# Optimization experiments

Measured on AMD Instinct MI355X. Metric: run time of the kernel, lower is better.

## Reference

```python
import jax, jax.numpy as jnp
import numpy as np

B, S, H = 2, 2048, 2048
NH, G = 16, 4
HD = H // NH  # 128


def setup_inputs() -> dict:
    key = jax.random.key(0)
    ks = jax.random.split(key, 9)
    sc = 0.02
    x = jax.random.normal(ks[0], (B, S, H), dtype=jnp.float32)
    # causal mask: 1.0 where j > i (masked), added as mask * -1e9 (matches torch code)
    causal_mask = jnp.triu(jnp.ones((S, S), dtype=jnp.float32), k=1)[None, None]
    Wq = jax.random.normal(ks[1], (H, H), dtype=jnp.float32) * sc
    bq = jnp.zeros((H,), dtype=jnp.float32)
    Wk = jax.random.normal(ks[2], (H, G * HD), dtype=jnp.float32) * sc
    bk = jnp.zeros((G * HD,), dtype=jnp.float32)
    Wv = jax.random.normal(ks[3], (H, G * HD), dtype=jnp.float32) * sc
    bv = jnp.zeros((G * HD,), dtype=jnp.float32)
    Wo = jax.random.normal(ks[4], (H, H), dtype=jnp.float32) * sc
    bo = jnp.zeros((H,), dtype=jnp.float32)
    return {"hidden_state": x, "causal_mask": causal_mask,
            "Wq": Wq, "bq": bq, "Wk": Wk, "bk": bk,
            "Wv": Wv, "bv": bv, "Wo": Wo, "bo": bo}


def reference(hidden_state, causal_mask, Wq, bq, Wk, bk, Wv, bv, Wo, bo):
    bsz, seq_len, _ = hidden_state.shape
    npg = NH // G  # query heads per KV group
    q = hidden_state @ Wq + bq                      # [B,S,H]
    k = hidden_state @ Wk + bk                      # [B,S,G*HD]
    v = hidden_state @ Wv + bv                      # [B,S,G*HD]
    # split heads; group query heads by KV group instead of repeating K/V
    q = q.reshape(bsz, seq_len, G, npg, HD).transpose(0, 2, 3, 1, 4)   # [B,G,npg,S,HD]
    k = k.reshape(bsz, seq_len, G, HD).transpose(0, 2, 1, 3)           # [B,G,S,HD]
    v = v.reshape(bsz, seq_len, G, HD).transpose(0, 2, 1, 3)           # [B,G,S,HD]
    scale = 1.0 / jnp.sqrt(jnp.float32(HD))
    scores = jnp.einsum('bgnsd,bgtd->bgnst', q, k) * scale             # [B,G,npg,S,S]
    scores = scores + causal_mask[:, :, None] * (-1e9)
    probs = jax.nn.softmax(scores, axis=-1)
    out = jnp.einsum('bgnst,bgtd->bgnsd', probs, v)                    # [B,G,npg,S,HD]
    out = out.transpose(0, 3, 1, 2, 4).reshape(bsz, seq_len, H)        # [B,S,H]
    return out @ Wo + bo
```

## Files before the change

### kernel.cpp

```cpp
#include <hip/hip_runtime.h>
#include <hip/hip_bf16.h>

#define B_   2
#define S_   2048
#define H_   2048
#define NH_  16
#define G_   4
#define HD_  128
#define NPG_ 4
#define MROWS_ (B_ * S_)
#define KVC_   (G_ * HD_)
#define NT_    (S_ / 64)
#define QSCALE_ 0.08838834764831845f

typedef __attribute__((ext_vector_type(8))) short bf16x8;
typedef __attribute__((ext_vector_type(4))) float f32x4;

__device__ __forceinline__ short f2bf_s(float f) {
    __hip_bfloat16 h = __float2bfloat16(f);
    short s; __builtin_memcpy(&s, &h, 2); return s;
}

__device__ __forceinline__ void gll16(const void* g, void* l) {
    __builtin_amdgcn_global_load_lds(
        (const __attribute__((address_space(1))) unsigned int*)g,
        (__attribute__((address_space(3))) unsigned int*)l, 16, 0, 0);
}

struct alignas(16) bf8pack { short s[8]; };
struct alignas(8)  s4pack  { short s[4]; };

__device__ __forceinline__ bf16x8 ld2x64(const short* p) {
    s4pack lo = *(const s4pack*)p;
    s4pack hi = *(const s4pack*)(p + 4);
    bf16x8 v;
    __builtin_memcpy(&v, &lo, 8);
    __builtin_memcpy((char*)&v + 8, &hi, 8);
    return v;
}

__device__ __forceinline__ void tile_transpose(
    const float* __restrict__ in, __hip_bfloat16* __restrict__ out,
    int R, int C, int bx, int by, int tid) {
    __shared__ short tile[32][33];
    int tx = tid & 31, ty0 = tid >> 5;
    #pragma unroll
    for (int i = 0; i < 32; i += 8)
        tile[ty0 + i][tx] = f2bf_s(in[(size_t)(by * 32 + ty0 + i) * C + bx * 32 + tx]);
    __syncthreads();
    #pragma unroll
    for (int i = 0; i < 32; i += 8) {
        short s = tile[tx][ty0 + i];
        __hip_bfloat16 h; __builtin_memcpy(&h, &s, 2);
        out[(size_t)(bx * 32 + ty0 + i) * R + by * 32 + tx] = h;
    }
}

__global__ __launch_bounds__(256) void prep(
    const float* __restrict__ x,  bf8pack* __restrict__ xb,
    const float* __restrict__ Wq, __hip_bfloat16* __restrict__ WqT,
    const float* __restrict__ Wk, __hip_bfloat16* __restrict__ WkT,
    const float* __restrict__ Wv, __hip_bfloat16* __restrict__ WvT,
    const float* __restrict__ Wo, __hip_bfloat16* __restrict__ WoT,
    const float* __restrict__ bq, const float* __restrict__ bk,
    const float* __restrict__ bv, float* __restrict__ bqkv) {
    const int bid = blockIdx.x, tid = threadIdx.x;
    if (bid < 4096) {
        int i = bid * 256 + tid;
        const float4* p = (const float4*)(x + (size_t)i * 8);
        float4 a = p[0], c = p[1];
        bf8pack o;
        o.s[0] = f2bf_s(a.x); o.s[1] = f2bf_s(a.y);
        o.s[2] = f2bf_s(a.z); o.s[3] = f2bf_s(a.w);
        o.s[4] = f2bf_s(c.x); o.s[5] = f2bf_s(c.y);
        o.s[6] = f2bf_s(c.z); o.s[7] = f2bf_s(c.w);
        xb[i] = o;
    } else if (bid < 8192) {
        int t = bid - 4096;
        tile_transpose(Wq, WqT, H_, H_, t & 63, t >> 6, tid);
    } else if (bid < 9216) {
        int t = bid - 8192;
        tile_transpose(Wk, WkT, H_, KVC_, t & 15, t >> 4, tid);
    } else if (bid < 10240) {
        int t = bid - 9216;
        tile_transpose(Wv, WvT, H_, KVC_, t & 15, t >> 4, tid);
    } else if (bid < 14336) {
        int t = bid - 10240;
        tile_transpose(Wo, WoT, H_, H_, t & 63, t >> 6, tid);
    } else {
        int i = (bid - 14336) * 256 + tid;
        if (i < 3072)
            bqkv[i] = (i < 2048) ? bq[i] : (i < 2560) ? bk[i - 2048] : bv[i - 2560];
    }
}

#define GEMM_STAGE(As_, Bs_, Ap_, Bp_, K_)                                   \
    {                                                                        \
        const int lrow = lane >> 3;                                          \
        const int cg = ((lane ^ lrow) & 7) * 8;                              \
        _Pragma("unroll")                                                    \
        for (int p = 0; p < 4; ++p) {                                        \
            int r0 = wave * 32 + p * 8;                                      \
            gll16(Ap_ + (size_t)(bm + r0 + lrow) * K_ + kt + cg,             \
                  &As_[r0 * 64]);                                            \
            gll16(Bp_ + (size_t)(bn + r0 + lrow) * K_ + kt + cg,             \
                  &Bs_[r0 * 64]);                                            \
        }                                                                    \
    }

#define GEMM_MFMA(As_, Bs_)                                                  \
    _Pragma("unroll")                                                        \
    for (int ks = 0; ks < 2; ++ks) {                                         \
        bf16x8 af[4], bfr[4];                                                \
        _Pragma("unroll")                                                    \
        for (int i = 0; i < 4; ++i) {                                        \
            int ra = wm + i * 16 + l15, rb = wn + i * 16 + l15;              \
            af[i]  = *(const bf16x8*)(&As_[ra * 64 +                         \
                          (((ks * 4 + quad) ^ (ra & 7)) * 8)]);              \
            bfr[i] = *(const bf16x8*)(&Bs_[rb * 64 +                         \
                          (((ks * 4 + quad) ^ (rb & 7)) * 8)]);              \
        }                                                                    \
        _Pragma("unroll")                                                    \
        for (int i = 0; i < 4; ++i)                                          \
            _Pragma("unroll")                                                \
            for (int j = 0; j < 4; ++j)                                      \
                acc[i][j] = __builtin_amdgcn_mfma_f32_16x16x32_bf16(         \
                    af[i], bfr[j], acc[i][j], 0, 0, 0);                      \
    }

__global__ __launch_bounds__(256) void gemm_qkv(
    const __hip_bfloat16* __restrict__ A,
    const __hip_bfloat16* __restrict__ Bt,
    const float* __restrict__ bias,
    __hip_bfloat16* __restrict__ Qo,
    __hip_bfloat16* __restrict__ Ko,
    __hip_bfloat16* __restrict__ VtG) {
    __shared__ short As[128 * 64];
    __shared__ short Bs[128 * 64];
    const int K = H_;
    const int t = threadIdx.x;
    const int lane = t & 63, wave = t >> 6;
    const int l15 = lane & 15, quad = lane >> 4;
    const int bm = blockIdx.x * 128, bn = blockIdx.y * 128;
    const int wm = (wave >> 1) * 64, wn = (wave & 1) * 64;

    f32x4 acc[4][4] = {};
    for (int kt = 0; kt < K; kt += 64) {
        GEMM_STAGE(As, Bs, A, Bt, K)
        __syncthreads();
        GEMM_MFMA(As, Bs)
        __syncthreads();
    }

    if (bn < 2560) {
        __hip_bfloat16* Cp; int stride, cb; float scl;
        if (bn < 2048) { Cp = Qo; stride = H_;   cb = bn;        scl = QSCALE_; }
        else           { Cp = Ko; stride = KVC_; cb = bn - 2048; scl = 1.f; }
        #pragma unroll
        for (int i = 0; i < 4; ++i) {
            int row0 = bm + wm + i * 16 + quad * 4;
            #pragma unroll
            for (int j = 0; j < 4; ++j) {
                int colg = bn + wn + j * 16 + l15;
                int coll = cb + wn + j * 16 + l15;
                float bv = bias[colg];
                #pragma unroll
                for (int r = 0; r < 4; ++r)
                    Cp[(size_t)(row0 + r) * stride + coll] =
                        __float2bfloat16((acc[i][j][r] + bv) * scl);
            }
        }
    } else {
        #pragma unroll
        for (int i = 0; i < 4; ++i) {
            int row0 = bm + wm + i * 16 + quad * 4;
            #pragma unroll
            for (int j = 0; j < 4; ++j) {
                int colg = bn + wn + j * 16 + l15;
                int coll = colg - 2560;
                float bv = bias[colg];
                short s4[4];
                #pragma unroll
                for (int r = 0; r < 4; ++r) s4[r] = f2bf_s(acc[i][j][r] + bv);
                *(uint2*)(&VtG[(size_t)coll * MROWS_ + row0]) = *(uint2*)s4;
            }
        }
    }
}

__global__ __launch_bounds__(256) void gemm_out(
    const __hip_bfloat16* __restrict__ A,
    const __hip_bfloat16* __restrict__ Bt,
    const float* __restrict__ bias,
    float* __restrict__ C) {
    __shared__ short As[128 * 64];
    __shared__ short Bs[128 * 64];
    const int K = H_, N = H_;
    const int t = threadIdx.x;
    const int lane = t & 63, wave = t >> 6;
    const int l15 = lane & 15, quad = lane >> 4;
    const int bm = blockIdx.x * 128, bn = blockIdx.y * 128;
    const int wm = (wave >> 1) * 64, wn = (wave & 1) * 64;

    f32x4 acc[4][4] = {};
    for (int kt = 0; kt < K; kt += 64) {
        GEMM_STAGE(As, Bs, A, Bt, K)
        __syncthreads();
        GEMM_MFMA(As, Bs)
        __syncthreads();
    }

    #pragma unroll
    for (int i = 0; i < 4; ++i) {
        int row0 = bm + wm + i * 16 + quad * 4;
        #pragma unroll
        for (int j = 0; j < 4; ++j) {
            int col = bn + wn + j * 16 + l15;
            float bv = bias[col];
            #pragma unroll
            for (int r = 0; r < 4; ++r)
                C[(size_t)(row0 + r) * N + col] = acc[i][j][r] + bv;
        }
    }
}

__global__ __launch_bounds__(256, 2) void attn_causal_gqa(
    const __hip_bfloat16* __restrict__ Q,
    const __hip_bfloat16* __restrict__ K,
    const __hip_bfloat16* __restrict__ VtG,
    __hip_bfloat16* __restrict__ O) {
    __shared__ short KsL[64 * 128];
    __shared__ short VtL[128 * 64];
    __shared__ short Ps[4][2][16 * 72];

    const int h  = blockIdx.x;
    const int b  = h >> 4;
    const int hh = h & 15;
    const int g  = hh >> 2;
    const int qb1 = blockIdx.y;
    const int qb2 = NT_ - 1 - qb1;

    const int t = threadIdx.x;
    const int lane = t & 63, wave = t >> 6;
    const int l15 = lane & 15, quad = lane >> 4;
    const int swz = l15 & 7;

    const __hip_bfloat16* Qb = Q + (size_t)b * S_ * H_ + hh * HD_;
    const __hip_bfloat16* Kb = K + (size_t)b * S_ * KVC_ + g * HD_;
    const __hip_bfloat16* Vg = VtG + (size_t)g * HD_ * MROWS_ + b * S_;

    bf16x8 aq1[4], aq2[4];
    {
        const int qr1 = qb1 * 64 + wave * 16 + l15;
        const int qr2 = qb2 * 64 + wave * 16 + l15;
        #pragma unroll
        for (int kk = 0; kk < 4; ++kk) {
            aq1[kk] = *(const bf16x8*)(Qb + (size_t)qr1 * H_ + kk * 32 + quad * 8);
            aq2[kk] = *(const bf16x8*)(Qb + (size_t)qr2 * H_ + kk * 32 + quad * 8);
        }
    }

    f32x4 o1[8] = {}, o2[8] = {};
    float lp1 = 0.f, lp2 = 0.f;
    const int qrow_loc = wave * 16 + l15;

    for (int tile = 0; tile <= qb2; ++tile) {
        const int key0 = tile * 64;
        const bool do1 = (tile <= qb1);

        #pragma unroll
        for (int p = 0; p < 4; ++p) {
            int R0 = wave * 16 + p * 4;
            int row = R0 + (lane >> 4);
            int cg = ((lane & 15) ^ (row & 7)) * 8;
            gll16(Kb + (size_t)(key0 + row) * KVC_ + cg, &KsL[R0 * 128]);
        }
        #pragma unroll
        for (int p = 0; p < 4; ++p) {
            int R0 = wave * 32 + p * 8;
            int row = R0 + (lane >> 3);
            int cg = ((lane & 7) ^ (row & 7)) * 8;
            gll16(Vg + (size_t)row * MROWS_ + key0 + cg, &VtL[R0 * 64]);
        }
        __syncthreads();

        f32x4 s2[4] = {}, s1[4] = {};
        #pragma unroll
        for (int kk = 0; kk < 4; ++kk) {
            bf16x8 bk[4];
            #pragma unroll
            for (int nt = 0; nt < 4; ++nt)
                bk[nt] = *(const bf16x8*)(
                    &KsL[(nt * 16 + l15) * 128 + (((kk * 4 + quad) ^ swz) * 8)]);
            #pragma unroll
            for (int nt = 0; nt < 4; ++nt)
                s2[nt] = __builtin_amdgcn_mfma_f32_16x16x32_bf16(
                    bk[nt], aq2[kk], s2[nt], 0, 0, 0);
            if (do1) {
                #pragma unroll
                for (int nt = 0; nt < 4; ++nt)
                    s1[nt] = __builtin_amdgcn_mfma_f32_16x16x32_bf16(
                        bk[nt], aq1[kk], s1[nt], 0, 0, 0);
            }
        }

        __asm__ volatile("" ::: "memory");
        short* P2 = &Ps[wave][1][0];
        {
            const bool m2 = (tile == qb2);
            #pragma unroll
            for (int nt = 0; nt < 4; ++nt) {
                s4pack pk;
                #pragma unroll
                for (int r = 0; r < 4; ++r) {
                    float p = __expf(s2[nt][r]);
                    if (m2 && (nt * 16 + quad * 4 + r > qrow_loc)) p = 0.f;
                    lp2 += p;
                    pk.s[r] = f2bf_s(p);
                }
                *(s4pack*)&P2[l15 * 72 + nt * 16 + quad * 4] = pk;
            }
        }
        short* P1 = &Ps[wave][0][0];
        if (do1) {
            const bool m1 = (tile == qb1);
            #pragma unroll
            for (int nt = 0; nt < 4; ++nt) {
                s4pack pk;
                #pragma unroll
                for (int r = 0; r < 4; ++r) {
                    float p = __expf(s1[nt][r]);
                    if (m1 && (nt * 16 + quad * 4 + r > qrow_loc)) p = 0.f;
                    lp1 += p;
                    pk.s[r] = f2bf_s(p);
                }
                *(s4pack*)&P1[l15 * 72 + nt * 16 + quad * 4] = pk;
            }
        }
        __asm__ volatile("" ::: "memory");

        #pragma unroll
        for (int ks = 0; ks < 2; ++ks) {
            bf16x8 ap2 = ld2x64(&P2[l15 * 72 + ks * 32 + quad * 8]);
            bf16x8 ap1;
            if (do1) ap1 = ld2x64(&P1[l15 * 72 + ks * 32 + quad * 8]);
            #pragma unroll
            for (int n2 = 0; n2 < 8; ++n2) {
                bf16x8 bv = *(const bf16x8*)(
                    &VtL[(n2 * 16 + l15) * 64 + (((ks * 4 + quad) ^ swz) * 8)]);
                o2[n2] = __builtin_amdgcn_mfma_f32_16x16x32_bf16(
                    ap2, bv, o2[n2], 0, 0, 0);
                if (do1)
                    o1[n2] = __builtin_amdgcn_mfma_f32_16x16x32_bf16(
                        ap1, bv, o1[n2], 0, 0, 0);
            }
        }
        __syncthreads();
    }

    float L1 = lp1, L2 = lp2;
    L1 += __shfl_xor(L1, 16); L2 += __shfl_xor(L2, 16);
    L1 += __shfl_xor(L1, 32); L2 += __shfl_xor(L2, 32);
    #pragma unroll
    for (int r = 0; r < 4; ++r) {
        float i1 = 1.f / __shfl(L1, quad * 4 + r);
        float i2 = 1.f / __shfl(L2, quad * 4 + r);
        int s1r = qb1 * 64 + wave * 16 + quad * 4 + r;
        int s2r = qb2 * 64 + wave * 16 + quad * 4 + r;
        #pragma unroll
        for (int n2 = 0; n2 < 8; ++n2) {
            int d = n2 * 16 + l15;
            O[((size_t)b * S_ + s1r) * H_ + hh * HD_ + d] = __float2bfloat16(o1[n2][r] * i1);
            O[((size_t)b * S_ + s2r) * H_ + hh * HD_ + d] = __float2bfloat16(o2[n2][r] * i2);
        }
    }
}

extern "C" void kernel_launch(void* const* d_in, const int* in_sizes, int n_in,
                              void* d_out, int out_size, void* d_ws, size_t ws_size,
                              hipStream_t stream) {
    const float* x  = (const float*)d_in[0];
    const float* Wq = (const float*)d_in[2];
    const float* bq = (const float*)d_in[3];
    const float* Wk = (const float*)d_in[4];
    const float* bk = (const float*)d_in[5];
    const float* Wv = (const float*)d_in[6];
    const float* bv = (const float*)d_in[7];
    const float* Wo = (const float*)d_in[8];
    const float* bo = (const float*)d_in[9];
    float* out = (float*)d_out;

    char* ws = (char*)d_ws;
    const size_t MB = 1024 * 1024;
    __hip_bfloat16* xb   = (__hip_bfloat16*)(ws);
    __hip_bfloat16* WT   = (__hip_bfloat16*)(ws + 16 * MB);
    __hip_bfloat16* Kws  = (__hip_bfloat16*)(ws + 28 * MB);
    __hip_bfloat16* VtG  = (__hip_bfloat16*)(ws + 32 * MB);
    __hip_bfloat16* WoT  = (__hip_bfloat16*)(ws + 36 * MB);
    float*          bqkv = (float*)         (ws + 44 * MB);
    __hip_bfloat16* Aws  = (__hip_bfloat16*)(ws);
    __hip_bfloat16* Qbuf = (__hip_bfloat16*)d_out;

    prep<<<14348, 256, 0, stream>>>(
        x, (bf8pack*)xb,
        Wq, WT,
        Wk, WT + (size_t)2048 * H_,
        Wv, WT + (size_t)2560 * H_,
        Wo, WoT,
        bq, bk, bv, bqkv);

    gemm_qkv<<<dim3(MROWS_ / 128, 3072 / 128), 256, 0, stream>>>(
        xb, WT, bqkv, Qbuf, Kws, VtG);

    attn_causal_gqa<<<dim3(B_ * NH_, NT_ / 2), 256, 0, stream>>>(Qbuf, Kws, VtG, Aws);

    gemm_out<<<dim3(MROWS_ / 128, H_ / 128), 256, 0, stream>>>(Aws, WoT, bo, out);
}
```

Baseline: 315.5 us.

## Rewrite projection GEMMs as 8-wave double-buffered pipelined kernels with larger tiles

Replaces the 128x128, 4-wave, single-buffered QKV and output GEMMs with 8-wave (512-thread) kernels using 256x256 and 128x256 tiles. LDS is double-buffered and the next k-tile's global-to-LDS loads are interleaved between four MFMA phases, with explicit vmcnt waits, raw barriers and setprio. This aims to hide load latency and raise arithmetic intensity per block. In exchange it uses much more LDS and registers per block, and it launches fewer blocks (192 for QKV, 256 for the output GEMM), which may underfill the GPU.

```diff
diff --git a/kernel.cpp b/kernel.cpp
--- a/kernel.cpp
+++ b/kernel.cpp
@@ -94,70 +94,140 @@
     }
 }
 
-#define GEMM_STAGE(As_, Bs_, Ap_, Bp_, K_)                                   \
-    {                                                                        \
-        const int lrow = lane >> 3;                                          \
-        const int cg = ((lane ^ lrow) & 7) * 8;                              \
-        _Pragma("unroll")                                                    \
-        for (int p = 0; p < 4; ++p) {                                        \
-            int r0 = wave * 32 + p * 8;                                      \
-            gll16(Ap_ + (size_t)(bm + r0 + lrow) * K_ + kt + cg,             \
-                  &As_[r0 * 64]);                                            \
-            gll16(Bp_ + (size_t)(bn + r0 + lrow) * K_ + kt + cg,             \
-                  &Bs_[r0 * 64]);                                            \
-        }                                                                    \
-    }
-
-#define GEMM_MFMA(As_, Bs_)                                                  \
-    _Pragma("unroll")                                                        \
-    for (int ks = 0; ks < 2; ++ks) {                                         \
-        bf16x8 af[4], bfr[4];                                                \
-        _Pragma("unroll")                                                    \
-        for (int i = 0; i < 4; ++i) {                                        \
-            int ra = wm + i * 16 + l15, rb = wn + i * 16 + l15;              \
-            af[i]  = *(const bf16x8*)(&As_[ra * 64 +                         \
-                          (((ks * 4 + quad) ^ (ra & 7)) * 8)]);              \
-            bfr[i] = *(const bf16x8*)(&Bs_[rb * 64 +                         \
-                          (((ks * 4 + quad) ^ (rb & 7)) * 8)]);              \
-        }                                                                    \
-        _Pragma("unroll")                                                    \
-        for (int i = 0; i < 4; ++i)                                          \
-            _Pragma("unroll")                                                \
-            for (int j = 0; j < 4; ++j)                                      \
-                acc[i][j] = __builtin_amdgcn_mfma_f32_16x16x32_bf16(         \
-                    af[i], bfr[j], acc[i][j], 0, 0, 0);                      \
-    }
-
-__global__ __launch_bounds__(256) void gemm_qkv(
+#define PHASE8(QM, QN)                                                        \
+    {                                                                         \
+        bf16x8 af[2][MH], bfr[2][2];                                          \
+        _Pragma("unroll")                                                     \
+        for (int ks = 0; ks < 2; ++ks) {                                      \
+            _Pragma("unroll")                                                 \
+            for (int ii = 0; ii < MH; ++ii) {                                 \
+                const int ra = wm + ((QM) * MH + ii) * 16 + l15;              \
+                af[ks][ii] = *(const bf16x8*)(Ab + ra * 64 +                  \
+                    (((ks * 4 + quad) ^ (ra & 7)) << 3));                     \
+            }                                                                 \
+            _Pragma("unroll")                                                 \
+            for (int jj = 0; jj < 2; ++jj) {                                  \
+                const int rb = wn + ((QN) * 2 + jj) * 16 + l15;               \
+                bfr[ks][jj] = *(const bf16x8*)(Bb + rb * 64 +                 \
+                    (((ks * 4 + quad) ^ (rb & 7)) << 3));                     \
+            }                                                                 \
+        }                                                                     \
+        asm volatile("s_barrier" ::: "memory");                               \
+        __builtin_amdgcn_s_setprio(1);                                        \
+        _Pragma("unroll")                                                     \
+        for (int ks = 0; ks < 2; ++ks)                                        \
+            _Pragma("unroll")                                                 \
+            for (int ii = 0; ii < MH; ++ii)                                   \
+                _Pragma("unroll")                                             \
+                for (int jj = 0; jj < 2; ++jj)                                \
+                    acc[(QM) * MH + ii][(QN) * 2 + jj] =                      \
+                        __builtin_amdgcn_mfma_f32_16x16x32_bf16(              \
+                            af[ks][ii], bfr[ks][jj],                          \
+                            acc[(QM) * MH + ii][(QN) * 2 + jj], 0, 0, 0);     \
+        __builtin_amdgcn_s_setprio(0);                                        \
+        asm volatile("s_barrier" ::: "memory");                               \
+    }
+
+template <int BM>
+__device__ __forceinline__ void gemm8p(
+    const __hip_bfloat16* __restrict__ A,
+    const __hip_bfloat16* __restrict__ Bt,
+    const int K, const int bm, const int bn,
+    short* __restrict__ As, short* __restrict__ Bs,
+    f32x4 (* __restrict__ acc)[4])
+{
+    constexpr int MF  = BM / 32;
+    constexpr int MH  = MF / 2;
+    constexpr int AI  = BM / 64;
+    constexpr int ASZ = BM * 64;
+    constexpr int BSZ = 256 * 64;
+    const int t = threadIdx.x;
+    const int lane = t & 63, wave = t >> 6;
+    const int l15 = lane & 15, quad = lane >> 4;
+    const int lrow = lane >> 3, lcg = lane & 7;
+    const int wm = (wave >> 2) * (BM / 2);
+    const int wn = (wave & 3) * 64;
+    const int nt = K >> 6;
+
+    auto stageA = [&](int ti, int b) {
+        const int kt = ti << 6;
+        short* Ad = As + b * ASZ;
+        #pragma unroll
+        for (int p = 0; p < AI; ++p) {
+            const int r0 = wave * (AI * 8) + p * 8;
+            const int row = r0 + lrow;
+            gll16(A + (size_t)(bm + row) * K + kt + ((lcg ^ (row & 7)) << 3),
+                  Ad + r0 * 64);
+        }
+    };
+    auto stageB = [&](int ti, int b) {
+        const int kt = ti << 6;
+        short* Bd = Bs + b * BSZ;
+        #pragma unroll
+        for (int p = 0; p < 4; ++p) {
+            const int r0 = wave * 32 + p * 8;
+            const int row = r0 + lrow;
+            gll16(Bt + (size_t)(bn + row) * K + kt + ((lcg ^ (row & 7)) << 3),
+                  Bd + r0 * 64);
+        }
+    };
+
+    stageA(0, 0); stageB(0, 0);
+    stageA(1, 1); stageB(1, 1);
+
+    for (int ti = 0; ti < nt; ++ti) {
+        const int b = ti & 1;
+        const short* Ab = As + b * ASZ;
+        const short* Bb = Bs + b * BSZ;
+        const bool pf = (ti + 2 < nt);
+
+        if (ti == nt - 1) {
+            asm volatile("s_waitcnt vmcnt(0)" ::: "memory");
+        } else if constexpr (BM == 256) {
+            asm volatile("s_waitcnt vmcnt(8)" ::: "memory");
+        } else {
+            asm volatile("s_waitcnt vmcnt(6)" ::: "memory");
+        }
+        asm volatile("s_barrier" ::: "memory");
+
+        PHASE8(0, 0)
+        PHASE8(0, 1)
+        if (pf && (wave & 3) < 2) stageA(ti + 2, b);
+        PHASE8(1, 0)
+        if (pf && !(wave & 1)) stageB(ti + 2, b);
+        PHASE8(1, 1)
+        if (pf) {
+            if ((wave & 3) >= 2) stageA(ti + 2, b);
+            if (wave & 1) stageB(ti + 2, b);
+        }
+    }
+}
+
+__global__ __launch_bounds__(512, 2) void gemm_qkv8(
     const __hip_bfloat16* __restrict__ A,
     const __hip_bfloat16* __restrict__ Bt,
     const float* __restrict__ bias,
     __hip_bfloat16* __restrict__ Qo,
     __hip_bfloat16* __restrict__ Ko,
     __hip_bfloat16* __restrict__ VtG) {
-    __shared__ short As[128 * 64];
-    __shared__ short Bs[128 * 64];
-    const int K = H_;
+    __shared__ __align__(16) short As[2 * 256 * 64];
+    __shared__ __align__(16) short Bs[2 * 256 * 64];
+    const int bm = blockIdx.x * 256, bn = blockIdx.y * 256;
+
+    f32x4 acc[8][4] = {};
+    gemm8p<256>(A, Bt, H_, bm, bn, As, Bs, acc);
+
     const int t = threadIdx.x;
     const int lane = t & 63, wave = t >> 6;
     const int l15 = lane & 15, quad = lane >> 4;
-    const int bm = blockIdx.x * 128, bn = blockIdx.y * 128;
-    const int wm = (wave >> 1) * 64, wn = (wave & 1) * 64;
-
-    f32x4 acc[4][4] = {};
-    for (int kt = 0; kt < K; kt += 64) {
-        GEMM_STAGE(As, Bs, A, Bt, K)
-        __syncthreads();
-        GEMM_MFMA(As, Bs)
-        __syncthreads();
-    }
+    const int wm = (wave >> 2) * 128, wn = (wave & 3) * 64;
 
     if (bn < 2560) {
         __hip_bfloat16* Cp; int stride, cb; float scl;
         if (bn < 2048) { Cp = Qo; stride = H_;   cb = bn;        scl = QSCALE_; }
         else           { Cp = Ko; stride = KVC_; cb = bn - 2048; scl = 1.f; }
         #pragma unroll
-        for (int i = 0; i < 4; ++i) {
+        for (int i = 0; i < 8; ++i) {
             int row0 = bm + wm + i * 16 + quad * 4;
             #pragma unroll
             for (int j = 0; j < 4; ++j) {
@@ -172,43 +242,38 @@
         }
     } else {
         #pragma unroll
-        for (int i = 0; i < 4; ++i) {
+        for (int i = 0; i < 8; ++i) {
             int row0 = bm + wm + i * 16 + quad * 4;
             #pragma unroll
             for (int j = 0; j < 4; ++j) {
                 int colg = bn + wn + j * 16 + l15;
                 int coll = colg - 2560;
                 float bv = bias[colg];
-                short s4[4];
+                short s4v[4];
                 #pragma unroll
-                for (int r = 0; r < 4; ++r) s4[r] = f2bf_s(acc[i][j][r] + bv);
-                *(uint2*)(&VtG[(size_t)coll * MROWS_ + row0]) = *(uint2*)s4;
-            }
-        }
-    }
-}
-
-__global__ __launch_bounds__(256) void gemm_out(
+                for (int r = 0; r < 4; ++r) s4v[r] = f2bf_s(acc[i][j][r] + bv);
+                *(uint2*)(&VtG[(size_t)coll * MROWS_ + row0]) = *(uint2*)s4v;
+            }
+        }
+    }
+}
+
+__global__ __launch_bounds__(512, 2) void gemm_out8(
     const __hip_bfloat16* __restrict__ A,
     const __hip_bfloat16* __restrict__ Bt,
     const float* __restrict__ bias,
     float* __restrict__ C) {
-    __shared__ short As[128 * 64];
-    __shared__ short Bs[128 * 64];
-    const int K = H_, N = H_;
+    __shared__ __align__(16) short As[2 * 128 * 64];
+    __shared__ __align__(16) short Bs[2 * 256 * 64];
+    const int bm = blockIdx.x * 128, bn = blockIdx.y * 256;
+
+    f32x4 acc[4][4] = {};
+    gemm8p<128>(A, Bt, H_, bm, bn, As, Bs, acc);
+
     const int t = threadIdx.x;
     const int lane = t & 63, wave = t >> 6;
     const int l15 = lane & 15, quad = lane >> 4;
-    const int bm = blockIdx.x * 128, bn = blockIdx.y * 128;
-    const int wm = (wave >> 1) * 64, wn = (wave & 1) * 64;
-
-    f32x4 acc[4][4] = {};
-    for (int kt = 0; kt < K; kt += 64) {
-        GEMM_STAGE(As, Bs, A, Bt, K)
-        __syncthreads();
-        GEMM_MFMA(As, Bs)
-        __syncthreads();
-    }
+    const int wm = (wave >> 2) * 64, wn = (wave & 3) * 64;
 
     #pragma unroll
     for (int i = 0; i < 4; ++i) {
@@ -219,7 +284,7 @@
             float bv = bias[col];
             #pragma unroll
             for (int r = 0; r < 4; ++r)
-                C[(size_t)(row0 + r) * N + col] = acc[i][j][r] + bv;
+                C[(size_t)(row0 + r) * H_ + col] = acc[i][j][r] + bv;
         }
     }
 }
@@ -409,10 +474,10 @@
         Wo, WoT,
         bq, bk, bv, bqkv);
 
-    gemm_qkv<<<dim3(MROWS_ / 128, 3072 / 128), 256, 0, stream>>>(
+    gemm_qkv8<<<dim3(MROWS_ / 256, 3072 / 256), 512, 0, stream>>>(
         xb, WT, bqkv, Qbuf, Kws, VtG);
 
     attn_causal_gqa<<<dim3(B_ * NH_, NT_ / 2), 256, 0, stream>>>(Qbuf, Kws, VtG, Aws);
 
-    gemm_out<<<dim3(MROWS_ / 128, H_ / 128), 256, 0, stream>>>(Aws, WoT, bo, out);
-}
+    gemm_out8<<<dim3(MROWS_ / 128, H_ / 256), 512, 0, stream>>>(Aws, WoT, bo, out);
+}
```

Result: slower. 365.1 us (+15.7%).
